# Kernel optimization log

Hardware: AMD Instinct MI355X
Metric: run time of the kernel (lower is better)

## Reference

```python
import jax, jax.numpy as jnp
import numpy as np

IN, OUT, RANK, ALPHA, NSUB = 4096, 4096, 16, 32, 4
SCALING = ALPHA / RANK


def setup_inputs() -> dict:
    key = jax.random.key(0)
    ks = jax.random.split(key, 8)
    B, S = 4, 2048
    return {
        "x": jax.random.normal(ks[0], (B, S, IN), dtype=jnp.float32),
        "base_W": jax.random.normal(ks[1], (OUT, IN), dtype=jnp.float32) * 0.02,
        "base_b": jax.random.normal(ks[2], (OUT,), dtype=jnp.float32) * 0.02,
        "base_A": jax.random.normal(ks[3], (RANK, IN), dtype=jnp.float32) * 0.02,
        "base_B": jax.random.normal(ks[4], (OUT, RANK), dtype=jnp.float32) * 0.02,
        "sub_wgate": jax.random.normal(ks[5], (NSUB, IN), dtype=jnp.float32) * 0.02,
        "sub_A": jax.random.normal(ks[6], (NSUB, RANK, IN), dtype=jnp.float32) * 0.02,
        "sub_B": jax.random.normal(ks[7], (NSUB, OUT, RANK), dtype=jnp.float32) * 0.02,
    }


def reference(x, base_W, base_b, base_A, base_B, sub_wgate, sub_A, sub_B):
    # base linear: [B,S,IN] @ [IN,OUT] + bias
    out = jnp.einsum("bsd,od->bso", x, base_W) + base_b
    # base LoRA: x @ A^T @ B^T
    out = out + SCALING * jnp.einsum("bsr,or->bso", jnp.einsum("bsd,rd->bsr", x, base_A), base_B)
    # stacked ReLU-gated sub-adapters, batched over adapter dim j
    gates = jax.nn.relu(jnp.einsum("bsd,jd->bsj", x, sub_wgate))        # [B,S,J]
    mid = jnp.einsum("bsd,jrd->bsjr", x, sub_A)                           # [B,S,J,R] (small)
    # gate * (mid @ B^T) == (gate*mid) @ B^T since gate is per-token scalar
    gated_mid = mid * gates[..., None]
    out = out + SCALING * jnp.einsum("bsjr,jor->bso", gated_mid, sub_B)
    return out
```

## Files before the change

### kernel.cpp

```cpp
#include <hip/hip_runtime.h>
#include <hip/hip_bf16.h>
#include <stdint.h>

#define DIN   4096
#define DOUT  4096
#define RANK  16
#define NSUB  4
#define MTOT  8192
#define LDK   4160
#define KTAIL 64
#define NV    80

typedef __attribute__((ext_vector_type(8)))  short    short8;
typedef __attribute__((ext_vector_type(4)))  float    floatx4;
typedef __attribute__((ext_vector_type(8)))  unsigned short ushort8;
typedef __attribute__((ext_vector_type(4)))  unsigned short ushort4v;

static __device__ __forceinline__ unsigned short f2bf(float f) {
    unsigned int u = __float_as_uint(f);
    unsigned int r = (u + 0x7FFFu + ((u >> 16) & 1u)) >> 16;
    return (unsigned short)r;
}

static __device__ __forceinline__ void async_copy16(const unsigned short* g, unsigned short* l) {
    __builtin_amdgcn_global_load_lds(
        (const __attribute__((address_space(1))) unsigned int*)g,
        (__attribute__((address_space(3))) unsigned int*)l,
        16, 0, 0);
}

__global__ __launch_bounds__(256) void build_v_kernel(
    const float* __restrict__ sub_wgate,
    const float* __restrict__ sub_A,
    unsigned short* __restrict__ Vc)
{
    const int t = threadIdx.x;
    const int row = blockIdx.x;
    const float* src = (row < 64) ? (sub_A + (size_t)row * DIN)
                     : (row < 68) ? (sub_wgate + (size_t)(row - 64) * DIN)
                     : nullptr;
#pragma unroll
    for (int i = 0; i < 4; ++i) {
        int c4 = t + 256 * i;
        ushort4v v;
        if (src) {
            float4 a = ((const float4*)src)[c4];
            v[0] = f2bf(a.x); v[1] = f2bf(a.y); v[2] = f2bf(a.z); v[3] = f2bf(a.w);
        } else {
            v[0] = v[1] = v[2] = v[3] = 0;
        }
        *(ushort4v*)(Vc + (size_t)row * DIN + c4 * 4) = v;
    }
}

#define BXK 256
#define LDA 264
__global__ __launch_bounds__(256) void build_x_kernel(
    const float* __restrict__ x,
    const unsigned short* __restrict__ Vc,
    unsigned short* __restrict__ Xc)
{
    __shared__ char smem[(16 + NV) * LDA * 2];
    unsigned short* As = (unsigned short*)smem;
    unsigned short* Bs = As + 16 * LDA;
    float* Pp = (float*)smem;

    const int t  = threadIdx.x;
    const int l  = t & 63;
    const int w  = t >> 6;
    const int m0 = blockIdx.x * 16;
    const int lane16 = l & 15;
    const int kq     = (l >> 4) * 8;

    floatx4 acc[5] = {};

    for (int cc = 0; cc < DIN; cc += BXK) {
#pragma unroll
        for (int i = 0; i < 2; ++i) {
            int u8 = t + 256 * i;
            int tr = u8 >> 5;
            int c8 = u8 & 31;
            const float4* src = (const float4*)(x + (size_t)(m0 + tr) * DIN + cc + c8 * 8);
            float4 a = src[0], b = src[1];
            ushort8 v;
            v[0] = f2bf(a.x); v[1] = f2bf(a.y); v[2] = f2bf(a.z); v[3] = f2bf(a.w);
            v[4] = f2bf(b.x); v[5] = f2bf(b.y); v[6] = f2bf(b.z); v[7] = f2bf(b.w);
            *(ushort8*)&As[tr * LDA + c8 * 8] = v;
            *(ushort8*)(Xc + (size_t)(m0 + tr) * LDK + cc + c8 * 8) = v;
        }
#pragma unroll
        for (int i = 0; i < 10; ++i) {
            int idx = t + 256 * i;
            int vr  = idx >> 5;
            int c8  = idx & 31;
            ushort8 v = *(const ushort8*)(Vc + (size_t)vr * DIN + cc + c8 * 8);
            *(ushort8*)&Bs[vr * LDA + c8 * 8] = v;
        }
        __syncthreads();

#pragma unroll
        for (int s = 0; s < 2; ++s) {
            int ks = w * 2 + s;
            short8 af = *(const short8*)&As[lane16 * LDA + ks * 32 + kq];
#pragma unroll
            for (int n = 0; n < 5; ++n) {
                short8 bf = *(const short8*)&Bs[(n * 16 + lane16) * LDA + ks * 32 + kq];
                acc[n] = __builtin_amdgcn_mfma_f32_16x16x32_bf16(af, bf, acc[n], 0, 0, 0);
            }
        }
        __syncthreads();
    }

#pragma unroll
    for (int n = 0; n < 5; ++n)
#pragma unroll
        for (int r = 0; r < 4; ++r)
            Pp[(w * 16 + (l >> 4) * 4 + r) * NV + n * 16 + lane16] = acc[n][r];
    __syncthreads();

#pragma unroll
    for (int i = 0; i < 4; ++i) {
        int v  = t + 256 * i;
        int tr = v >> 6;
        int c  = v & 63;
        int j  = c >> 4;
        float ps = 0.f, gs = 0.f;
#pragma unroll
        for (int q = 0; q < 4; ++q) {
            ps += Pp[(q * 16 + tr) * NV + c];
            gs += Pp[(q * 16 + tr) * NV + 64 + j];
        }
        Xc[(size_t)(m0 + tr) * LDK + DIN + c] = f2bf(2.0f * fmaxf(gs, 0.f) * ps);
    }
}

__global__ __launch_bounds__(256) void build_w_kernel(
    const float* __restrict__ W,
    const float* __restrict__ base_A,
    const float* __restrict__ base_B,
    const float* __restrict__ sub_B,
    unsigned short* __restrict__ Wc)
{
    __shared__ float bBs[8 * RANK];

    const int t  = threadIdx.x;
    const int o0 = (blockIdx.x >> 2) * 8;
    const int cc = (blockIdx.x & 3) * 1024;
    const int q  = (cc >> 2) + t;

    if (t < 128) bBs[t] = 2.0f * base_B[(size_t)o0 * RANK + t];
    __syncthreads();

    float4 acc[8];
#pragma unroll
    for (int o = 0; o < 8; ++o)
        acc[o] = ((const float4*)(W + (size_t)(o0 + o) * DIN))[q];

#pragma unroll
    for (int r = 0; r < RANK; ++r) {
        float4 a = ((const float4*)(base_A + (size_t)r * DIN))[q];
#pragma unroll
        for (int o = 0; o < 8; ++o) {
            float s = bBs[o * RANK + r];
            acc[o].x += s * a.x; acc[o].y += s * a.y;
            acc[o].z += s * a.z; acc[o].w += s * a.w;
        }
    }

#pragma unroll
    for (int o = 0; o < 8; ++o) {
        ushort4v v;
        v[0] = f2bf(acc[o].x); v[1] = f2bf(acc[o].y);
        v[2] = f2bf(acc[o].z); v[3] = f2bf(acc[o].w);
        *(ushort4v*)(Wc + (size_t)(o0 + o) * LDK + q * 4) = v;
    }

    if ((blockIdx.x & 3) == 0) {
#pragma unroll
        for (int i = 0; i < 2; ++i) {
            int v = t + 256 * i;
            int o = v >> 6;
            int c = v & 63;
            int j = c >> 4;
            int r = c & 15;
            float s = sub_B[((size_t)j * DOUT + (o0 + o)) * RANK + r];
            Wc[(size_t)(o0 + o) * LDK + DIN + c] = f2bf(s);
        }
    }
}

__global__ __launch_bounds__(256) void gemm_kernel(
    const unsigned short* __restrict__ Xc,
    const unsigned short* __restrict__ Wc,
    const float* __restrict__ bias,
    float* __restrict__ out)
{
    __shared__ unsigned short As[128 * 32];
    __shared__ unsigned short Bs[128 * 32];

    const int t  = threadIdx.x;
    const int l  = t & 63;
    const int w  = t >> 6;
    const int wm = w >> 1;
    const int wn = w & 1;
    const int m0 = blockIdx.y * 128;
    const int n0 = blockIdx.x * 128;

    floatx4 acc[4][4] = {};

    const int srow = t >> 2;
    const int skc  = (t & 3) * 8;
    const unsigned short* gA = Xc + (size_t)(m0 + srow) * LDK + skc;
    const unsigned short* gB = Wc + (size_t)(n0 + srow) * LDK + skc;
    unsigned short* lA = &As[t * 8];
    unsigned short* lB = &Bs[t * 8];

    const int kq   = (l >> 4) * 8;
    const int lane16 = l & 15;

    for (int kk = 0; kk < LDK; kk += 32) {
        async_copy16(gA + kk, lA);
        async_copy16(gA + kk + (size_t)64 * LDK, lA + 64 * 32);
        async_copy16(gB + kk, lB);
        async_copy16(gB + kk + (size_t)64 * LDK, lB + 64 * 32);
        __syncthreads();

        short8 af[4], bf[4];
#pragma unroll
        for (int i = 0; i < 4; ++i) {
            af[i] = *(const short8*)&As[(wm * 64 + i * 16 + lane16) * 32 + kq];
            bf[i] = *(const short8*)&Bs[(wn * 64 + i * 16 + lane16) * 32 + kq];
        }
#pragma unroll
        for (int i = 0; i < 4; ++i)
#pragma unroll
            for (int j = 0; j < 4; ++j)
                acc[i][j] = __builtin_amdgcn_mfma_f32_16x16x32_bf16(af[i], bf[j], acc[i][j], 0, 0, 0);
        __syncthreads();
    }

    const int row_l = (l >> 4) * 4;
#pragma unroll
    for (int j = 0; j < 4; ++j) {
        int gcol = n0 + wn * 64 + j * 16 + lane16;
        float bv = bias[gcol];
#pragma unroll
        for (int i = 0; i < 4; ++i) {
            int grow = m0 + wm * 64 + i * 16 + row_l;
            size_t base = (size_t)grow * DOUT + gcol;
            out[base]            = acc[i][j][0] + bv;
            out[base + DOUT]     = acc[i][j][1] + bv;
            out[base + 2 * DOUT] = acc[i][j][2] + bv;
            out[base + 3 * DOUT] = acc[i][j][3] + bv;
        }
    }
}

extern "C" void kernel_launch(void* const* d_in, const int* in_sizes, int n_in,
                              void* d_out, int out_size, void* d_ws, size_t ws_size,
                              hipStream_t stream) {
    const float* x         = (const float*)d_in[0];
    const float* base_W    = (const float*)d_in[1];
    const float* base_b    = (const float*)d_in[2];
    const float* base_A    = (const float*)d_in[3];
    const float* base_B    = (const float*)d_in[4];
    const float* sub_wgate = (const float*)d_in[5];
    const float* sub_A     = (const float*)d_in[6];
    const float* sub_B     = (const float*)d_in[7];
    float* out = (float*)d_out;

    unsigned short* Xc = (unsigned short*)d_ws;
    unsigned short* Wc = Xc + (size_t)MTOT * LDK;
    unsigned short* Vc = Wc + (size_t)DOUT * LDK;

    build_v_kernel<<<NV, 256, 0, stream>>>(sub_wgate, sub_A, Vc);
    build_x_kernel<<<MTOT / 16, 256, 0, stream>>>(x, Vc, Xc);
    build_w_kernel<<<(DOUT / 8) * 4, 256, 0, stream>>>(base_W, base_A, base_B, sub_B, Wc);
    gemm_kernel<<<dim3(DOUT / 128, MTOT / 128), 256, 0, stream>>>(Xc, Wc, base_b, out);
}
```

Measured before the change: 627.8 us.

## Rewrite GEMM as 256x256 tile, 8-wave, double-buffered pipelined MFMA kernel

Replaces the simple 128x128 single-buffered GEMM with a 256x256 tile per 512-thread block that uses a 128KB LDS double buffer, with XOR-swizzled LDS layout. Global-to-LDS async copies for upcoming k-tiles are interleaved with four MFMA phases per iteration, using barriers, waitcnt and setprio to overlap load and compute. Blocks are remapped in a grouped order to improve L2 reuse. The cost is high LDS use that limits occupancy, plus manual synchronisation that is fragile.

```diff
diff --git a/kernel.cpp b/kernel.cpp
--- a/kernel.cpp
+++ b/kernel.cpp
@@ -10,6 +10,7 @@
 #define LDK   4160
 #define KTAIL 64
 #define NV    80
+#define KTILES 65
 
 typedef __attribute__((ext_vector_type(8)))  short    short8;
 typedef __attribute__((ext_vector_type(4)))  float    floatx4;
@@ -189,64 +190,138 @@
     }
 }
 
-__global__ __launch_bounds__(256) void gemm_kernel(
+#define STAGE_A(tt, h, b) do { \
+    const unsigned short* s_ = gA + (size_t)(h) * 128 * LDK + (tt) * 64; \
+    unsigned short* d_ = &lds[((b) << 14) + (h) * 8192 + tid * 8]; \
+    async_copy16(s_, d_); \
+    async_copy16(s_ + (size_t)64 * LDK, d_ + 4096); \
+} while (0)
+
+#define STAGE_B(tt, h, b) do { \
+    const unsigned short* s_ = gB + (size_t)(h) * 128 * LDK + (tt) * 64; \
+    unsigned short* d_ = &lds[32768 + ((b) << 14) + (h) * 8192 + tid * 8]; \
+    async_copy16(s_, d_); \
+    async_copy16(s_ + (size_t)64 * LDK, d_ + 4096); \
+} while (0)
+
+#define LDA_(b, mh, i, s) (*(const short8*)&lds[((b) << 14) + \
+    (wm * 128 + (mh) * 64 + (i) * 16 + lane16) * 64 + ((((s) * 4 + g) ^ lx) << 3)])
+#define LDB_(b, j, s) (*(const short8*)&lds[32768 + ((b) << 14) + \
+    (wn * 64 + (j) * 16 + lane16) * 64 + ((((s) * 4 + g) ^ lx) << 3)])
+
+#define MFMA_QUAD(mh, jlo) do { \
+    _Pragma("unroll") \
+    for (int i_ = 0; i_ < 4; ++i_) { \
+        _Pragma("unroll") \
+        for (int jj_ = 0; jj_ < 2; ++jj_) { \
+            acc[(mh)*4+i_][(jlo)+jj_] = __builtin_amdgcn_mfma_f32_16x16x32_bf16( \
+                af[i_][0], bb[(jlo)+jj_][0], acc[(mh)*4+i_][(jlo)+jj_], 0, 0, 0); \
+            acc[(mh)*4+i_][(jlo)+jj_] = __builtin_amdgcn_mfma_f32_16x16x32_bf16( \
+                af[i_][1], bb[(jlo)+jj_][1], acc[(mh)*4+i_][(jlo)+jj_], 0, 0, 0); \
+        } \
+    } \
+} while (0)
+
+#define PH_SYNC() do { \
+    __builtin_amdgcn_s_barrier(); \
+    asm volatile("s_waitcnt lgkmcnt(0)" ::: "memory"); \
+    __builtin_amdgcn_sched_barrier(0); \
+} while (0)
+
+__global__ __launch_bounds__(512, 2) void gemm_kernel(
     const unsigned short* __restrict__ Xc,
     const unsigned short* __restrict__ Wc,
     const float* __restrict__ bias,
     float* __restrict__ out)
 {
-    __shared__ unsigned short As[128 * 32];
-    __shared__ unsigned short Bs[128 * 32];
-
-    const int t  = threadIdx.x;
-    const int l  = t & 63;
-    const int w  = t >> 6;
-    const int wm = w >> 1;
-    const int wn = w & 1;
-    const int m0 = blockIdx.y * 128;
-    const int n0 = blockIdx.x * 128;
-
-    floatx4 acc[4][4] = {};
-
-    const int srow = t >> 2;
-    const int skc  = (t & 3) * 8;
-    const unsigned short* gA = Xc + (size_t)(m0 + srow) * LDK + skc;
-    const unsigned short* gB = Wc + (size_t)(n0 + srow) * LDK + skc;
-    unsigned short* lA = &As[t * 8];
-    unsigned short* lB = &Bs[t * 8];
-
-    const int kq   = (l >> 4) * 8;
+    __shared__ unsigned short lds[65536];
+
+    const int tid = threadIdx.x;
+    const int l   = tid & 63;
+    const int wv  = tid >> 6;
+    const int wm  = wv >> 2;
+    const int wn  = wv & 3;
     const int lane16 = l & 15;
-
-    for (int kk = 0; kk < LDK; kk += 32) {
-        async_copy16(gA + kk, lA);
-        async_copy16(gA + kk + (size_t)64 * LDK, lA + 64 * 32);
-        async_copy16(gB + kk, lB);
-        async_copy16(gB + kk + (size_t)64 * LDK, lB + 64 * 32);
-        __syncthreads();
-
-        short8 af[4], bf[4];
-#pragma unroll
-        for (int i = 0; i < 4; ++i) {
-            af[i] = *(const short8*)&As[(wm * 64 + i * 16 + lane16) * 32 + kq];
-            bf[i] = *(const short8*)&Bs[(wn * 64 + i * 16 + lane16) * 32 + kq];
-        }
-#pragma unroll
-        for (int i = 0; i < 4; ++i)
-#pragma unroll
-            for (int j = 0; j < 4; ++j)
-                acc[i][j] = __builtin_amdgcn_mfma_f32_16x16x32_bf16(af[i], bf[j], acc[i][j], 0, 0, 0);
-        __syncthreads();
-    }
-
-    const int row_l = (l >> 4) * 4;
+    const int g   = l >> 4;
+    const int lx  = lane16 & 7;
+
+    const int bid   = blockIdx.x;
+    const int wg    = (bid & 7) * 64 + (bid >> 3);
+    const int m0    = (wg >> 4) * 256;
+    const int n0    = (wg & 15) * 256;
+
+    const int r0 = tid >> 3;
+    const int c0 = (tid & 7) ^ (r0 & 7);
+    const unsigned short* gA = Xc + (size_t)(m0 + r0) * LDK + c0 * 8;
+    const unsigned short* gB = Wc + (size_t)(n0 + r0) * LDK + c0 * 8;
+
+    floatx4 acc[8][4] = {};
+    short8 af[4][2], bb[4][2];
+
+    STAGE_B(0, 0, 0); STAGE_B(0, 1, 0); STAGE_A(0, 0, 0); STAGE_A(0, 1, 0);
+    STAGE_B(1, 0, 1); STAGE_B(1, 1, 1); STAGE_A(1, 0, 1);
+    asm volatile("s_waitcnt vmcnt(6)" ::: "memory");
+    __builtin_amdgcn_s_barrier();
+
+    for (int t = 0; t < KTILES; ++t) {
+        const int cur = t & 1, nx = cur ^ 1;
+
+#pragma unroll
+        for (int i = 0; i < 4; ++i) { af[i][0] = LDA_(cur, 0, i, 0); af[i][1] = LDA_(cur, 0, i, 1); }
+        if (wn < 2) {
+#pragma unroll
+            for (int j = 0; j < 4; ++j) { bb[j][0] = LDB_(cur, j, 0); bb[j][1] = LDB_(cur, j, 1); }
+            asm volatile("" :: "v"(bb[2][0]), "v"(bb[2][1]), "v"(bb[3][0]), "v"(bb[3][1]));
+        } else {
+#pragma unroll
+            for (int j = 0; j < 2; ++j) { bb[j][0] = LDB_(cur, j, 0); bb[j][1] = LDB_(cur, j, 1); }
+        }
+        if (t + 1 < KTILES) STAGE_A(t + 1, 1, nx);
+        PH_SYNC();
+        __builtin_amdgcn_s_setprio(1);
+        MFMA_QUAD(0, 0);
+        __builtin_amdgcn_s_setprio(0);
+        __builtin_amdgcn_s_barrier();
+
+        if (wn >= 2) {
+#pragma unroll
+            for (int j = 2; j < 4; ++j) { bb[j][0] = LDB_(cur, j, 0); bb[j][1] = LDB_(cur, j, 1); }
+        }
+        if (t + 2 < KTILES) STAGE_B(t + 2, 0, cur);
+        PH_SYNC();
+        __builtin_amdgcn_s_setprio(1);
+        MFMA_QUAD(0, 2);
+        __builtin_amdgcn_s_setprio(0);
+        __builtin_amdgcn_s_barrier();
+
+#pragma unroll
+        for (int i = 0; i < 4; ++i) { af[i][0] = LDA_(cur, 1, i, 0); af[i][1] = LDA_(cur, 1, i, 1); }
+        if (t + 2 < KTILES) STAGE_B(t + 2, 1, cur);
+        PH_SYNC();
+        __builtin_amdgcn_s_setprio(1);
+        MFMA_QUAD(1, 0);
+        __builtin_amdgcn_s_setprio(0);
+        __builtin_amdgcn_s_barrier();
+
+        if (t + 2 < KTILES) STAGE_A(t + 2, 0, cur);
+        __builtin_amdgcn_s_barrier();
+        __builtin_amdgcn_sched_barrier(0);
+        __builtin_amdgcn_s_setprio(1);
+        MFMA_QUAD(1, 2);
+        __builtin_amdgcn_s_setprio(0);
+        if (t + 2 < KTILES)      { asm volatile("s_waitcnt vmcnt(6)" ::: "memory"); }
+        else if (t + 1 < KTILES) { asm volatile("s_waitcnt vmcnt(0)" ::: "memory"); }
+        __builtin_amdgcn_s_barrier();
+    }
+
+    const int row_l = g * 4;
 #pragma unroll
     for (int j = 0; j < 4; ++j) {
-        int gcol = n0 + wn * 64 + j * 16 + lane16;
-        float bv = bias[gcol];
-#pragma unroll
-        for (int i = 0; i < 4; ++i) {
-            int grow = m0 + wm * 64 + i * 16 + row_l;
+        const int gcol = n0 + wn * 64 + j * 16 + lane16;
+        const float bv = bias[gcol];
+#pragma unroll
+        for (int i = 0; i < 8; ++i) {
+            const int grow = m0 + wm * 128 + i * 16 + row_l;
             size_t base = (size_t)grow * DOUT + gcol;
             out[base]            = acc[i][j][0] + bv;
             out[base + DOUT]     = acc[i][j][1] + bv;
@@ -276,5 +351,5 @@
     build_v_kernel<<<NV, 256, 0, stream>>>(sub_wgate, sub_A, Vc);
     build_x_kernel<<<MTOT / 16, 256, 0, stream>>>(x, Vc, Xc);
     build_w_kernel<<<(DOUT / 8) * 4, 256, 0, stream>>>(base_W, base_A, base_B, sub_B, Wc);
-    gemm_kernel<<<dim3(DOUT / 128, MTOT / 128), 256, 0, stream>>>(Xc, Wc, base_b, out);
-}
+    gemm_kernel<<<(MTOT / 256) * (DOUT / 256), 512, 0, stream>>>(Xc, Wc, base_b, out);
+}
```

New measurement: 539.7 us. 1.16x faster.

## Rewrite GEMM as 256x256 double-buffered pipelined kernel with swizzled LDS

Applied to the files above, without the earlier changes.

Replaces the simple 128x128 single-buffered bf16 GEMM with a 256x256 tile, 512-thread kernel that uses a 64-wide K step and double-buffered LDS. Global-to-LDS async loads are interleaved with the MFMA phases, and raw barriers plus vmcnt waits overlap memory with compute. The change also XOR-swizzles the LDS layout to avoid bank conflicts, remaps block IDs for L2 locality, and raises MFMA priority. The cost is heavy register pressure from 32 accumulators and hand-managed synchronisation that is fragile.

```diff
diff --git a/kernel.cpp b/kernel.cpp
--- a/kernel.cpp
+++ b/kernel.cpp
@@ -10,6 +10,7 @@
 #define LDK   4160
 #define KTAIL 64
 #define NV    80
+#define KTILES 65
 
 typedef __attribute__((ext_vector_type(8)))  short    short8;
 typedef __attribute__((ext_vector_type(4)))  float    floatx4;
@@ -189,64 +190,110 @@
     }
 }
 
-__global__ __launch_bounds__(256) void gemm_kernel(
+#define BARM() asm volatile("s_barrier" ::: "memory")
+
+#define LDA_(B,MH,I,S) (*(const short8*)((const char*)lds + (B)*32768 + (MH)*8192 + (I)*2048 + (aBy ^ ((S)*64))))
+#define LDB_(B,J,S)    (*(const short8*)((const char*)lds + 65536 + (B)*32768 + (J)*2048 + (bBy ^ ((S)*64))))
+
+#define STG(P, DST) do { async_copy16((P), (DST)); \
+                         async_copy16((P) + (size_t)64 * LDK, (DST) + 4096); } while (0)
+#define STAGE_A0(P,B) STG((P), &lds[(B)*16384 + tid*8])
+#define STAGE_A1(P,B) STG((P), &lds[(B)*16384 + 8192 + tid*8])
+#define STAGE_B0(P,B) STG((P), &lds[32768 + (B)*16384 + tid*8])
+#define STAGE_B1(P,B) STG((P), &lds[32768 + (B)*16384 + 8192 + tid*8])
+
+#define MFMA_HALF(MH, JLO) do { \
+    _Pragma("unroll") for (int s_ = 0; s_ < 2; ++s_) \
+    _Pragma("unroll") for (int i_ = 0; i_ < 4; ++i_) \
+    _Pragma("unroll") for (int jj_ = 0; jj_ < 2; ++jj_) \
+        acc[(MH)*4+i_][(JLO)+jj_] = __builtin_amdgcn_mfma_f32_16x16x32_bf16( \
+            af[i_][s_], bb[(JLO)+jj_][s_], acc[(MH)*4+i_][(JLO)+jj_], 0, 0, 0); \
+} while (0)
+
+#define TILE_BODY(T, CUR) do { \
+     \
+    _Pragma("unroll") for (int i_ = 0; i_ < 4; ++i_) { \
+        af[i_][0] = LDA_(CUR, 0, i_, 0); af[i_][1] = LDA_(CUR, 0, i_, 1); } \
+    _Pragma("unroll") for (int j_ = 0; j_ < 2; ++j_) { \
+        bb[j_][0] = LDB_(CUR, j_, 0); bb[j_][1] = LDB_(CUR, j_, 1); } \
+    if ((T) + 1 < KTILES) { STAGE_A1(pA1, (CUR) ^ 1); } \
+    pA1 += 64; \
+    __builtin_amdgcn_s_setprio(1); MFMA_HALF(0, 0); __builtin_amdgcn_s_setprio(0); \
+    BARM(); \
+     \
+    _Pragma("unroll") for (int j_ = 2; j_ < 4; ++j_) { \
+        bb[j_][0] = LDB_(CUR, j_, 0); bb[j_][1] = LDB_(CUR, j_, 1); } \
+    __builtin_amdgcn_s_setprio(1); MFMA_HALF(0, 2); __builtin_amdgcn_s_setprio(0); \
+    BARM(); \
+     \
+    _Pragma("unroll") for (int i_ = 0; i_ < 4; ++i_) { \
+        af[i_][0] = LDA_(CUR, 1, i_, 0); af[i_][1] = LDA_(CUR, 1, i_, 1); } \
+    if ((T) + 2 < KTILES) { STAGE_B0(pB0, CUR); STAGE_B1(pB1, CUR); } \
+    pB0 += 64; pB1 += 64; \
+    BARM(); \
+    if ((T) + 2 < KTILES) { STAGE_A0(pA0, CUR); } \
+    pA0 += 64; \
+    __builtin_amdgcn_s_setprio(1); MFMA_HALF(1, 0); MFMA_HALF(1, 2); __builtin_amdgcn_s_setprio(0); \
+    if ((T) + 2 < KTILES)      { asm volatile("s_waitcnt vmcnt(6)" ::: "memory"); } \
+    else if ((T) + 1 < KTILES) { asm volatile("s_waitcnt vmcnt(0)" ::: "memory"); } \
+    BARM(); \
+} while (0)
+
+__global__ __launch_bounds__(512, 2) void gemm_kernel(
     const unsigned short* __restrict__ Xc,
     const unsigned short* __restrict__ Wc,
     const float* __restrict__ bias,
     float* __restrict__ out)
 {
-    __shared__ unsigned short As[128 * 32];
-    __shared__ unsigned short Bs[128 * 32];
-
-    const int t  = threadIdx.x;
-    const int l  = t & 63;
-    const int w  = t >> 6;
-    const int wm = w >> 1;
-    const int wn = w & 1;
-    const int m0 = blockIdx.y * 128;
-    const int n0 = blockIdx.x * 128;
-
-    floatx4 acc[4][4] = {};
-
-    const int srow = t >> 2;
-    const int skc  = (t & 3) * 8;
-    const unsigned short* gA = Xc + (size_t)(m0 + srow) * LDK + skc;
-    const unsigned short* gB = Wc + (size_t)(n0 + srow) * LDK + skc;
-    unsigned short* lA = &As[t * 8];
-    unsigned short* lB = &Bs[t * 8];
-
-    const int kq   = (l >> 4) * 8;
+    __shared__ unsigned short lds[65536];
+
+    const int tid = threadIdx.x;
+    const int l   = tid & 63;
+    const int wv  = tid >> 6;
+    const int wm  = wv >> 2;
+    const int wn  = wv & 3;
     const int lane16 = l & 15;
-
-    for (int kk = 0; kk < LDK; kk += 32) {
-        async_copy16(gA + kk, lA);
-        async_copy16(gA + kk + (size_t)64 * LDK, lA + 64 * 32);
-        async_copy16(gB + kk, lB);
-        async_copy16(gB + kk + (size_t)64 * LDK, lB + 64 * 32);
-        __syncthreads();
-
-        short8 af[4], bf[4];
-#pragma unroll
-        for (int i = 0; i < 4; ++i) {
-            af[i] = *(const short8*)&As[(wm * 64 + i * 16 + lane16) * 32 + kq];
-            bf[i] = *(const short8*)&Bs[(wn * 64 + i * 16 + lane16) * 32 + kq];
-        }
-#pragma unroll
-        for (int i = 0; i < 4; ++i)
-#pragma unroll
-            for (int j = 0; j < 4; ++j)
-                acc[i][j] = __builtin_amdgcn_mfma_f32_16x16x32_bf16(af[i], bf[j], acc[i][j], 0, 0, 0);
-        __syncthreads();
-    }
-
-    const int row_l = (l >> 4) * 4;
+    const int g   = l >> 4;
+    const int lx  = lane16 & 7;
+
+    const int bid = blockIdx.x;
+    const int wg  = (bid & 7) * 64 + (bid >> 3);
+    const int m0  = (wg >> 4) * 256;
+    const int n0  = (wg & 15) * 256;
+
+    const int aBy = wm * 16384 + lane16 * 128 + ((g ^ lx) << 4);
+    const int bBy = wn * 8192  + lane16 * 128 + ((g ^ lx) << 4);
+
+    const int r0 = tid >> 3;
+    const int c0 = (tid & 7) ^ (r0 & 7);
+    const unsigned short* pA0 = Xc + (size_t)(m0 + r0) * LDK + c0 * 8;
+    const unsigned short* pA1 = pA0 + (size_t)128 * LDK;
+    const unsigned short* pB0 = Wc + (size_t)(n0 + r0) * LDK + c0 * 8;
+    const unsigned short* pB1 = pB0 + (size_t)128 * LDK;
+
+    floatx4 acc[8][4] = {};
+    short8 af[4][2], bb[4][2];
+
+    STAGE_B0(pB0, 0); STAGE_B1(pB1, 0); STAGE_A0(pA0, 0); STAGE_A1(pA1, 0);
+    STAGE_B0(pB0 + 64, 1); STAGE_B1(pB1 + 64, 1); STAGE_A0(pA0 + 64, 1);
+    pA1 += 64; pB0 += 128; pB1 += 128; pA0 += 128;
+    asm volatile("s_waitcnt vmcnt(6)" ::: "memory");
+    BARM();
+
+    for (int t = 0; t < KTILES - 1; t += 2) {
+        TILE_BODY(t, 0);
+        TILE_BODY(t + 1, 1);
+    }
+    TILE_BODY(KTILES - 1, 0);
+
+    const int row_l = g * 4;
 #pragma unroll
     for (int j = 0; j < 4; ++j) {
-        int gcol = n0 + wn * 64 + j * 16 + lane16;
-        float bv = bias[gcol];
-#pragma unroll
-        for (int i = 0; i < 4; ++i) {
-            int grow = m0 + wm * 64 + i * 16 + row_l;
+        const int gcol = n0 + wn * 64 + j * 16 + lane16;
+        const float bv = bias[gcol];
+#pragma unroll
+        for (int i = 0; i < 8; ++i) {
+            const int grow = m0 + wm * 128 + i * 16 + row_l;
             size_t base = (size_t)grow * DOUT + gcol;
             out[base]            = acc[i][j][0] + bv;
             out[base + DOUT]     = acc[i][j][1] + bv;
@@ -276,5 +323,5 @@
     build_v_kernel<<<NV, 256, 0, stream>>>(sub_wgate, sub_A, Vc);
     build_x_kernel<<<MTOT / 16, 256, 0, stream>>>(x, Vc, Xc);
     build_w_kernel<<<(DOUT / 8) * 4, 256, 0, stream>>>(base_W, base_A, base_B, sub_B, Wc);
-    gemm_kernel<<<dim3(DOUT / 128, MTOT / 128), 256, 0, stream>>>(Xc, Wc, base_b, out);
-}
+    gemm_kernel<<<dim3(DOUT / 256 * (MTOT / 256)), 512, 0, stream>>>(Xc, Wc, base_b, out);
+}
```

New measurement: 524.4 us. 1.2x faster.
